# Kernel optimization log

Hardware: AMD Instinct MI355X
Metric: run time of the kernel (lower is better)

Reference implementation:

```python
import jax, jax.numpy as jnp
import numpy as np

V, OOV, E, HE, HD, B, S, T = 50000, 100, 128, 256, 256, 32, 256, 16
NEG = -1e20


def lstm(x, W, U, b, h0, c0):
    # x: [B, L, F]; standard (Keras-style i,f,g,o) LSTM via scan over time
    def step(carry, xt):
        h, c = carry
        z = xt @ W + h @ U + b
        i, f, g, o = jnp.split(z, 4, axis=-1)
        c = jax.nn.sigmoid(f) * c + jax.nn.sigmoid(i) * jnp.tanh(g)
        h = jax.nn.sigmoid(o) * jnp.tanh(c)
        return (h, c), h
    (h, c), hs = jax.lax.scan(step, (h0, c0), jnp.swapaxes(x, 0, 1))
    return jnp.swapaxes(hs, 0, 1), h, c


def setup_inputs() -> dict:
    key = jax.random.key(0)
    ks = jax.random.split(key, 16)
    g = lambda i, shape: jax.random.normal(ks[i], shape, dtype=jnp.float32) * 0.05
    return {
        'x': jax.random.randint(ks[0], (B, S), 0, V),
        'x_with_oov': jax.random.randint(ks[1], (B, S), 0, V + OOV),
        'x_len': jax.random.randint(ks[2], (B,), 1, S + 1),
        'dec_x': jax.random.randint(ks[3], (B, T), 0, V),
        'embedding': g(4, (V, E)),
        'Wenc': g(5, (E, 4 * HE)), 'Uenc': g(6, (HE, 4 * HE)), 'benc': jnp.zeros(4 * HE, jnp.float32),
        'We2d': g(7, (HE, HD)), 'be2d': jnp.zeros(HD, jnp.float32),
        'Wdec': g(8, (E, 4 * HD)), 'Udec': g(9, (HD, 4 * HD)), 'bdec': jnp.zeros(4 * HD, jnp.float32),
        'Wattn': g(10, (HD, HE)),
        'Wout': g(11, (HE + HD, HD)), 'bout': jnp.zeros(HD, jnp.float32),
        'Wgen': g(12, (HD, V)),
        'Wcopy': g(13, (HE, HD)), 'bcopy': jnp.zeros(HD, jnp.float32),
    }


def reference(x, x_with_oov, x_len, dec_x, embedding, Wenc, Uenc, benc,
              We2d, be2d, Wdec, Udec, bdec, Wattn, Wout, bout, Wgen, Wcopy, bcopy):
    # Encoder (unidirectional; Keras encoder ignores mask in this branch)
    enc_out, eh, ec = lstm(embedding[x], Wenc, Uenc, benc,
                           jnp.zeros((B, HE), embedding.dtype), jnp.zeros((B, HE), embedding.dtype))
    # NOTE: source applies encoder2decoder_state to BOTH h and c (faithful)
    h0 = eh @ We2d + be2d
    c0 = ec @ We2d + be2d
    # Decoder LSTM
    dec_out, sh, sc = lstm(embedding[dec_x], Wdec, Udec, bdec, h0, c0)  # [B,T,HD]
    mask = jnp.arange(S)[None, :] < x_len[:, None]                      # [B,S]
    # Attention (score_mode='general')
    scores = jnp.einsum('bth,he,bse->bts', dec_out, Wattn, enc_out)     # [B,T,S]
    scores = jnp.where(mask[:, None, :], scores, NEG)
    aw = jax.nn.softmax(scores, axis=2)
    ctx = jnp.einsum('bts,bse->bte', aw, enc_out)                       # [B,T,HE]
    attn_out = jnp.tanh(jnp.concatenate([ctx, dec_out], axis=-1) @ Wout + bout)  # [B,T,HD]
    # Generation scores, padded with tiny constant over OOV slots
    gen = jnp.exp(attn_out @ Wgen)                                      # [B,T,V]
    gen = jnp.pad(gen, ((0, 0), (0, 0), (0, OOV)), constant_values=1e-10)
    # Copy scores over source positions, scattered into extended vocab
    copy_seq = jnp.einsum('bsh,bth->bts', jnp.tanh(enc_out @ Wcopy + bcopy), attn_out)
    copy_seq = jnp.exp(jnp.where(mask[:, None, :], copy_seq, NEG))      # [B,T,S]
    b_idx = jnp.arange(B)[:, None, None]
    t_idx = jnp.arange(T)[None, :, None]
    v_idx = x_with_oov[:, None, :]                                      # broadcast to [B,T,S]
    copy_vocab = jnp.zeros((B, T, V + OOV), gen.dtype).at[b_idx, t_idx, v_idx].add(copy_seq)
    total = gen + copy_vocab
    log_prob = jnp.log(total / jnp.sum(total, axis=2, keepdims=True))
    return log_prob, sh, sc
```

## Files before the change

kernel.cpp:

```cpp
#include <hip/hip_runtime.h>

#define V_   50000
#define OOV_ 100
#define VO_  50100
#define E_   128
#define HE_  256
#define HD_  256
#define B_   32
#define S_   256
#define T_   16

typedef _Float16 h2_t __attribute__((ext_vector_type(2)));
typedef __attribute__((ext_vector_type(8))) short bfrag_t;
typedef __attribute__((ext_vector_type(4))) float f32x4;
typedef unsigned short ushort_t;

union U32H2 { unsigned u; h2_t h; };
union FRAG  { uint4 u; bfrag_t s; };

static __device__ __forceinline__ float bf2f(unsigned short b) {
  return __uint_as_float(((unsigned)b) << 16);
}
static __device__ __forceinline__ unsigned short f2bf(float f) {
  unsigned u = __float_as_uint(f);
  unsigned r = (u + 0x7fffu + ((u >> 16) & 1u)) >> 16;
  return (unsigned short)r;
}
static __device__ __forceinline__ float sigm(float x) { return 1.f / (1.f + expf(-x)); }
static __device__ __forceinline__ float fast_sigm(float z) {
  float e = __builtin_amdgcn_exp2f(-1.442695041f * z);
  return __builtin_amdgcn_rcpf(1.f + e);
}
static __device__ __forceinline__ float fast_tanh(float z) {
  float e = __builtin_amdgcn_exp2f(-2.885390082f * z);
  return 2.f * __builtin_amdgcn_rcpf(1.f + e) - 1.f;
}

static __device__ __forceinline__ float dot2u(unsigned upair, unsigned hpairv, float acc) {
  U32H2 a; a.u = upair;
  U32H2 b; b.u = hpairv;
#if __has_builtin(__builtin_amdgcn_fdot2)
  return __builtin_amdgcn_fdot2(a.h, b.h, acc, false);
#else
  acc = fmaf((float)a.h.x, (float)b.h.x, acc);
  return fmaf((float)a.h.y, (float)b.h.y, acc);
#endif
}

__global__ __launch_bounds__(256) void mfma_gemm(
    const ushort_t* __restrict__ A, const ushort_t* __restrict__ Bt,
    const float* __restrict__ bias, float* __restrict__ C, ushort_t* __restrict__ Cbf,
    float* __restrict__ rsum, int M, int N, int K, int ldC, int act)
{
  const int w = threadIdx.x >> 6, lane = threadIdx.x & 63;
  const int m0 = blockIdx.y * 64 + w * 16;
  const int n0 = blockIdx.x * 64;
  const int l16 = lane & 15, lq = lane >> 4;
  f32x4 acc[4] = {f32x4{0,0,0,0}, f32x4{0,0,0,0}, f32x4{0,0,0,0}, f32x4{0,0,0,0}};
  for (int k0 = 0; k0 < K; k0 += 32) {
    FRAG a;
    a.u = *(const uint4*)(A + (size_t)(m0 + l16) * K + k0 + lq * 8);
#pragma unroll
    for (int ns = 0; ns < 4; ns++) {
      int n = n0 + ns * 16 + l16;
      int nc = n < N ? n : N - 1;
      FRAG bf;
      bf.u = *(const uint4*)(Bt + (size_t)nc * K + k0 + lq * 8);
      acc[ns] = __builtin_amdgcn_mfma_f32_16x16x32_bf16(a.s, bf.s, acc[ns], 0, 0, 0);
    }
  }
  float bv[4];
#pragma unroll
  for (int ns = 0; ns < 4; ns++) {
    int col = n0 + ns * 16 + l16;
    bv[ns] = (bias && col < N) ? bias[col] : 0.f;
  }
#pragma unroll
  for (int r = 0; r < 4; r++) {
    int row = m0 + lq * 4 + r;
    float part = 0.f;
#pragma unroll
    for (int ns = 0; ns < 4; ns++) {
      int col = n0 + ns * 16 + l16;
      if (col < N) {
        float v = acc[ns][r] + bv[ns];
        if (act == 1) v = tanhf(v);
        else if (act == 2) v = expf(v);
        if (Cbf) Cbf[(size_t)row * ldC + col] = f2bf(v);
        else     C[(size_t)row * ldC + col] = v;
        part += v;
      }
    }
    if (rsum) {
      part += __shfl_xor(part, 1);
      part += __shfl_xor(part, 2);
      part += __shfl_xor(part, 4);
      part += __shfl_xor(part, 8);
      if (l16 == 0) atomicAdd(&rsum[row], part);
    }
  }
}

__global__ __launch_bounds__(256) void wgen_gemm(
    const ushort_t* __restrict__ A, const float* __restrict__ Wg,
    float* __restrict__ out, float* __restrict__ rsum)
{
  __shared__ ushort_t ldsB[64 * 264];
  const int tid = threadIdx.x;
  const int n0 = blockIdx.x * 64;
#pragma unroll
  for (int it = 0; it < 16; it++) {
    int idx = it * 256 + tid;
    int k = idx >> 4, c4 = idx & 15;
    int nsrc = n0 + c4 * 4;
    if (nsrc > V_ - 4) nsrc = V_ - 4;
    float4 f = *(const float4*)&Wg[(size_t)k * V_ + nsrc];
    ldsB[(c4 * 4 + 0) * 264 + k] = f2bf(f.x);
    ldsB[(c4 * 4 + 1) * 264 + k] = f2bf(f.y);
    ldsB[(c4 * 4 + 2) * 264 + k] = f2bf(f.z);
    ldsB[(c4 * 4 + 3) * 264 + k] = f2bf(f.w);
  }
  __syncthreads();
  const int w = tid >> 6, lane = tid & 63;
  const int l16 = lane & 15, lq = lane >> 4;
  for (int mt = 0; mt < 8; mt++) {
    const int mb = mt * 64 + w * 16;
    f32x4 acc[4] = {f32x4{0,0,0,0}, f32x4{0,0,0,0}, f32x4{0,0,0,0}, f32x4{0,0,0,0}};
#pragma unroll
    for (int k0 = 0; k0 < 256; k0 += 32) {
      FRAG a;
      a.u = *(const uint4*)(A + (size_t)(mb + l16) * 256 + k0 + lq * 8);
#pragma unroll
      for (int ns = 0; ns < 4; ns++) {
        FRAG bf;
        bf.u = *(const uint4*)&ldsB[(ns * 16 + l16) * 264 + k0 + lq * 8];
        acc[ns] = __builtin_amdgcn_mfma_f32_16x16x32_bf16(a.s, bf.s, acc[ns], 0, 0, 0);
      }
    }
#pragma unroll
    for (int r = 0; r < 4; r++) {
      int row = mb + lq * 4 + r;
      float part = 0.f;
#pragma unroll
      for (int ns = 0; ns < 4; ns++) {
        int col = n0 + ns * 16 + l16;
        if (col < V_) {
          float v = expf(acc[ns][r]);
          out[(size_t)row * VO_ + col] = v;
          part += v;
        }
      }
      part += __shfl_xor(part, 1);
      part += __shfl_xor(part, 2);
      part += __shfl_xor(part, 4);
      part += __shfl_xor(part, 8);
      if (l16 == 0) atomicAdd(&rsum[row], part);
    }
  }
}

static __device__ __forceinline__ void tconv_tile(
    const float* __restrict__ W, ushort_t* __restrict__ Wt, int K, int N,
    int kb, int nb, int tid, ushort_t (*tile)[33])
{
  const int tx = tid & 31, ty = tid >> 5;
#pragma unroll
  for (int p = 0; p < 4; p++) {
    int k = kb + ty + p * 8, n = nb + tx;
    if (k < K && n < N) tile[ty + p * 8][tx] = f2bf(W[(size_t)k * N + n]);
  }
  __syncthreads();
#pragma unroll
  for (int p = 0; p < 4; p++) {
    int n = nb + ty + p * 8, k = kb + tx;
    if (k < K && n < N) Wt[(size_t)n * K + k] = tile[tx][ty + p * 8];
  }
}
static __device__ __forceinline__ void packU2_one(
    const float* __restrict__ U, unsigned* __restrict__ out, int i)
{
  int p = i >> 10, col = i & 1023;
  U32H2 cv; cv.h = h2_t{(_Float16)U[(size_t)(2 * p) * 1024 + col],
                        (_Float16)U[(size_t)(2 * p + 1) * 1024 + col]};
  out[i] = cv.u;
}

__global__ __launch_bounds__(256) void prep_kernel(
    const float* __restrict__ Wenc, const float* __restrict__ Wdec,
    const float* __restrict__ We2d, const float* __restrict__ Wattn,
    const float* __restrict__ Wout, const float* __restrict__ Wcopy,
    const float* __restrict__ Uenc, const float* __restrict__ Udec,
    const int* __restrict__ x, const int* __restrict__ decx, const float* __restrict__ emb,
    ushort_t* WencT, ushort_t* WdecT, ushort_t* We2dT, ushort_t* WattnT,
    ushort_t* WoutT, ushort_t* WcopyT, unsigned* Upk2E, unsigned* Upk2D,
    ushort_t* xembbf, ushort_t* dembbf)
{
  __shared__ ushort_t tile[32][33];
  int blk = blockIdx.x;
  const int tid = threadIdx.x;
  if (blk < 128) { tconv_tile(Wenc, WencT, 128, 1024, (blk >> 5) * 32, (blk & 31) * 32, tid, tile); return; }
  blk -= 128;
  if (blk < 128) { tconv_tile(Wdec, WdecT, 128, 1024, (blk >> 5) * 32, (blk & 31) * 32, tid, tile); return; }
  blk -= 128;
  if (blk < 64)  { tconv_tile(We2d, We2dT, 256, 256, (blk >> 3) * 32, (blk & 7) * 32, tid, tile); return; }
  blk -= 64;
  if (blk < 64)  { tconv_tile(Wattn, WattnT, 256, 256, (blk >> 3) * 32, (blk & 7) * 32, tid, tile); return; }
  blk -= 64;
  if (blk < 128) { tconv_tile(Wout, WoutT, 512, 256, (blk >> 3) * 32, (blk & 7) * 32, tid, tile); return; }
  blk -= 128;
  if (blk < 64)  { tconv_tile(Wcopy, WcopyT, 256, 256, (blk >> 3) * 32, (blk & 7) * 32, tid, tile); return; }
  blk -= 64;
  if (blk < 512) { packU2_one(Uenc, Upk2E, blk * 256 + tid); return; }
  blk -= 512;
  if (blk < 512) { packU2_one(Udec, Upk2D, blk * 256 + tid); return; }
  blk -= 512;
  if (blk < 4096) {
    int i = blk * 256 + tid, r = i >> 7;
    xembbf[i] = f2bf(emb[(size_t)x[r] * E_ + (i & 127)]);
    return;
  }
  blk -= 4096;
  {
    int i = blk * 256 + tid, r = i >> 7;
    dembbf[i] = f2bf(emb[(size_t)decx[r] * E_ + (i & 127)]);
  }
}

#define DOT8(u0, u1, hpi)                \
  acc[0] = dot2u(u0.x, hpi, acc[0]);     \
  acc[1] = dot2u(u0.y, hpi, acc[1]);     \
  acc[2] = dot2u(u0.z, hpi, acc[2]);     \
  acc[3] = dot2u(u0.w, hpi, acc[3]);     \
  acc[4] = dot2u(u1.x, hpi, acc[4]);     \
  acc[5] = dot2u(u1.y, hpi, acc[5]);     \
  acc[6] = dot2u(u1.z, hpi, acc[6]);     \
  acc[7] = dot2u(u1.w, hpi, acc[7]);

__global__
__attribute__((amdgpu_flat_work_group_size(1024, 1024), amdgpu_waves_per_eu(4, 4)))
void lstm12(
    const float* __restrict__ Xpre, const unsigned* __restrict__ Upk2,
    const float* __restrict__ h0, const float* __restrict__ c0,
    ushort_t* __restrict__ outH, float* __restrict__ hN, float* __restrict__ cN,
    ushort_t* __restrict__ hNbf, ushort_t* __restrict__ cNbf,
    int steps)
{
  __shared__ unsigned ldsU[8 * 4096];
  __shared__ float    zpart[4 * 1028];
  __shared__ unsigned hpair[8 * 20];
  const int tid = threadIdx.x;

  const int b = blockIdx.x;
  const int jg = tid >> 3, kq = tid & 7;

  uint4 Ur[24];
  const unsigned* ubase = Upk2 + jg * 8;
#pragma unroll
  for (int i = 0; i < 12; i++) {
    int p = kq * 16 + i;
    Ur[2 * i]     = *(const uint4*)(ubase + p * 1024);
    Ur[2 * i + 1] = *(const uint4*)(ubase + p * 1024 + 4);
  }
  {
    unsigned* myst = &ldsU[tid * 4];
#pragma unroll
    for (int i = 0; i < 4; i++) {
      int p = kq * 16 + 12 + i;
      uint4 q0 = *(const uint4*)(ubase + p * 1024);
      uint4 q1 = *(const uint4*)(ubase + p * 1024 + 4);
      *(uint4*)(myst + (2 * i) * 4096)     = q0;
      *(uint4*)(myst + (2 * i + 1) * 4096) = q1;
    }
  }
  float c = 0.f, hcur = 0.f;
  if (tid < 256) {
    c    = c0 ? c0[b * 256 + tid] : 0.f;
    hcur = h0 ? h0[b * 256 + tid] : 0.f;
  }
  if (tid < 128) {
    float a  = h0 ? h0[b * 256 + 2 * tid] : 0.f;
    float b2 = h0 ? h0[b * 256 + 2 * tid + 1] : 0.f;
    U32H2 cv; cv.h = h2_t{(_Float16)a, (_Float16)b2};
    hpair[(tid >> 4) * 20 + (tid & 15)] = cv.u;
  }
  __syncthreads();

  const float* xp = Xpre + (size_t)b * steps * 1024;
  const unsigned* myld = &ldsU[tid * 4];

  for (int t = 0; t < steps; t++) {
    float xq0 = 0.f, xq1 = 0.f, xq2 = 0.f, xq3 = 0.f;
    if (tid < 256) {
      const float* xr = xp + (size_t)t * 1024 + tid;
      xq0 = xr[0]; xq1 = xr[256]; xq2 = xr[512]; xq3 = xr[768];
    }
    float acc[8] = {0.f, 0.f, 0.f, 0.f, 0.f, 0.f, 0.f, 0.f};
    {
      uint4 hA = *(const uint4*)&hpair[kq * 20];
      DOT8(Ur[0], Ur[1], hA.x)  DOT8(Ur[2], Ur[3], hA.y)
      DOT8(Ur[4], Ur[5], hA.z)  DOT8(Ur[6], Ur[7], hA.w)
    }
    {
      uint4 hB = *(const uint4*)&hpair[kq * 20 + 4];
      DOT8(Ur[8], Ur[9], hB.x)   DOT8(Ur[10], Ur[11], hB.y)
      DOT8(Ur[12], Ur[13], hB.z) DOT8(Ur[14], Ur[15], hB.w)
    }
    {
      uint4 hC = *(const uint4*)&hpair[kq * 20 + 8];
      DOT8(Ur[16], Ur[17], hC.x) DOT8(Ur[18], Ur[19], hC.y)
      DOT8(Ur[20], Ur[21], hC.z) DOT8(Ur[22], Ur[23], hC.w)
    }
    {
      uint4 hD = *(const uint4*)&hpair[kq * 20 + 12];
      unsigned hh[4] = {hD.x, hD.y, hD.z, hD.w};
#pragma unroll
      for (int r = 0; r < 4; r++) {
        uint4 u0 = *(const uint4*)(myld + (2 * r) * 4096);
        uint4 u1 = *(const uint4*)(myld + (2 * r + 1) * 4096);
        unsigned hpi = hh[r];
        DOT8(u0, u1, hpi)
      }
    }
#pragma unroll
    for (int g = 0; g < 8; g++) acc[g] += __shfl_xor(acc[g], 1);
    if ((kq & 1) == 0) {
      int r = kq >> 1;
      *(float4*)&zpart[r * 1028 + jg * 8]     = make_float4(acc[0], acc[1], acc[2], acc[3]);
      *(float4*)&zpart[r * 1028 + jg * 8 + 4] = make_float4(acc[4], acc[5], acc[6], acc[7]);
    }
    __syncthreads();
    if (tid < 256) {
      float zi = xq0, zf = xq1, zg = xq2, zo = xq3;
#pragma unroll
      for (int r = 0; r < 4; r++) {
        const float* zr = &zpart[r * 1028 + tid];
        zi += zr[0]; zf += zr[256]; zg += zr[512]; zo += zr[768];
      }
      float ai = fast_sigm(zi), af = fast_sigm(zf);
      float ag = fast_tanh(zg), ao = fast_sigm(zo);
      c = fmaf(af, c, ai * ag);
      hcur = ao * fast_tanh(c);
      outH[((size_t)b * steps + t) * 256 + tid] = f2bf(hcur);
      float hnx = __shfl_down(hcur, 1);
      if ((tid & 1) == 0) {
        U32H2 cv; cv.h = h2_t{(_Float16)hcur, (_Float16)hnx};
        int P = tid >> 1;
        hpair[(P >> 4) * 20 + (P & 15)] = cv.u;
      }
    }
    __syncthreads();
  }
  if (tid < 256) {
    if (hN)   hN[b * 256 + tid] = hcur;
    if (cN)   cN[b * 256 + tid] = c;
    if (hNbf) hNbf[b * 256 + tid] = f2bf(hcur);
    if (cNbf) cNbf[b * 256 + tid] = f2bf(c);
  }
}

__global__ __launch_bounds__(256) void attn_kernel(
    const float* __restrict__ dq, const ushort_t* __restrict__ enc,
    const int* __restrict__ x_len, const ushort_t* __restrict__ dec,
    ushort_t* __restrict__ catb)
{
  __shared__ float q[256];
  __shared__ float eb[32][256];
  __shared__ float sc[256];
  __shared__ float red[8];
  const int bt = blockIdx.x, tid = threadIdx.x;
  const int b = bt >> 4;
  q[tid] = dq[(size_t)bt * 256 + tid];
  const int len = x_len[b];
  const unsigned* encu = (const unsigned*)(enc + (size_t)b * S_ * 256);
  __syncthreads();
  const int s_loc = tid >> 3, hb = (tid & 7) * 32;
  for (int cch = 0; cch < 8; cch++) {
#pragma unroll
    for (int qv = 0; qv < 16; qv++) {
      int idx = qv * 256 + tid;
      unsigned u = encu[cch * 4096 + idx];
      int row = idx >> 7, cp2 = (idx & 127) * 2;
      eb[row][cp2]     = bf2f((unsigned short)(u & 0xffffu));
      eb[row][cp2 + 1] = bf2f((unsigned short)(u >> 16));
    }
    __syncthreads();
    float p = 0.f;
#pragma unroll
    for (int h = 0; h < 32; h++) p = fmaf(q[hb + h], eb[s_loc][hb + h], p);
    p += __shfl_down(p, 4, 8);
    p += __shfl_down(p, 2, 8);
    p += __shfl_down(p, 1, 8);
    if ((tid & 7) == 0) sc[cch * 32 + s_loc] = p;
    __syncthreads();
  }
  float my = (tid < len) ? sc[tid] : -1e30f;
  float m = my;
#pragma unroll
  for (int o = 32; o >= 1; o >>= 1) m = fmaxf(m, __shfl_xor(m, o));
  if ((tid & 63) == 0) red[tid >> 6] = m;
  __syncthreads();
  float bm = fmaxf(fmaxf(red[0], red[1]), fmaxf(red[2], red[3]));
  float e = expf(my - bm);
  float s = e;
#pragma unroll
  for (int o = 32; o >= 1; o >>= 1) s += __shfl_xor(s, o);
  if ((tid & 63) == 0) red[4 + (tid >> 6)] = s;
  __syncthreads();
  float tot = red[4] + red[5] + red[6] + red[7];
  sc[tid] = e / tot;
  __syncthreads();
  const ushort_t* encb = enc + (size_t)b * S_ * 256;
  float acc = 0.f;
  for (int s2 = 0; s2 < 256; s2++) acc = fmaf(sc[s2], bf2f(encb[(size_t)s2 * 256 + tid]), acc);
  catb[(size_t)bt * 512 + tid]       = f2bf(acc);
  catb[(size_t)bt * 512 + 256 + tid] = dec[(size_t)bt * 256 + tid];
}

__global__ __launch_bounds__(256) void copyseq_kernel(
    const ushort_t* __restrict__ at, const ushort_t* __restrict__ cp,
    const int* __restrict__ x_len, float* __restrict__ cseq)
{
  __shared__ float q[256];
  __shared__ float eb[32][256];
  __shared__ float sc[256];
  const int bt = blockIdx.x, tid = threadIdx.x;
  const int b = bt >> 4;
  q[tid] = bf2f(at[(size_t)bt * 256 + tid]);
  const int len = x_len[b];
  const unsigned* cpu_ = (const unsigned*)(cp + (size_t)b * S_ * 256);
  __syncthreads();
  const int s_loc = tid >> 3, hb = (tid & 7) * 32;
  for (int cch = 0; cch < 8; cch++) {
#pragma unroll
    for (int qv = 0; qv < 16; qv++) {
      int idx = qv * 256 + tid;
      unsigned u = cpu_[cch * 4096 + idx];
      int row = idx >> 7, cp2 = (idx & 127) * 2;
      eb[row][cp2]     = bf2f((unsigned short)(u & 0xffffu));
      eb[row][cp2 + 1] = bf2f((unsigned short)(u >> 16));
    }
    __syncthreads();
    float p = 0.f;
#pragma unroll
    for (int h = 0; h < 32; h++) p = fmaf(q[hb + h], eb[s_loc][hb + h], p);
    p += __shfl_down(p, 4, 8);
    p += __shfl_down(p, 2, 8);
    p += __shfl_down(p, 1, 8);
    if ((tid & 7) == 0) sc[cch * 32 + s_loc] = p;
    __syncthreads();
  }
  cseq[(size_t)bt * 256 + tid] = (tid < len) ? expf(sc[tid]) : 0.f;
}

__global__ __launch_bounds__(256) void scatter_kernel(
    const float* __restrict__ cseq, const int* __restrict__ xoov,
    float* __restrict__ out, float* __restrict__ rsum)
{
  __shared__ float red[4];
  const int bt = blockIdx.x, tid = threadIdx.x, b = bt >> 4;
  if (tid < OOV_) out[(size_t)bt * VO_ + V_ + tid] = 1e-10f;
  __syncthreads();
  float v = cseq[(size_t)bt * 256 + tid];
  if (v != 0.f) atomicAdd(&out[(size_t)bt * VO_ + xoov[b * S_ + tid]], v);
  float s = v;
#pragma unroll
  for (int o = 32; o >= 1; o >>= 1) s += __shfl_xor(s, o);
  if ((tid & 63) == 0) red[tid >> 6] = s;
  __syncthreads();
  if (tid == 0) atomicAdd(&rsum[bt], red[0] + red[1] + red[2] + red[3]);
}
__global__ void rowlog_kernel(const float* __restrict__ rsum, float* __restrict__ rowlog) {
  int i = blockIdx.x * 256 + threadIdx.x;
  if (i < B_ * T_) rowlog[i] = logf(rsum[i] + 1e-8f);
}
__global__ void finalize_kernel(float* __restrict__ out, const float* __restrict__ rowlog) {
  size_t i = (size_t)blockIdx.x * 256 + threadIdx.x;
  if (i < (size_t)B_ * T_ * VO_) {
    int bt = (int)(i / VO_);
    out[i] = logf(out[i]) - rowlog[bt];
  }
}

extern "C" void kernel_launch(void* const* d_in, const int* in_sizes, int n_in,
                              void* d_out, int out_size, void* d_ws, size_t ws_size,
                              hipStream_t stream) {
  const int*   x     = (const int*)d_in[0];
  const int*   xoov  = (const int*)d_in[1];
  const int*   xlen  = (const int*)d_in[2];
  const int*   decx  = (const int*)d_in[3];
  const float* emb   = (const float*)d_in[4];
  const float* Wenc  = (const float*)d_in[5];
  const float* Uenc  = (const float*)d_in[6];
  const float* benc  = (const float*)d_in[7];
  const float* We2d  = (const float*)d_in[8];
  const float* be2d  = (const float*)d_in[9];
  const float* Wdec  = (const float*)d_in[10];
  const float* Udec  = (const float*)d_in[11];
  const float* bdec  = (const float*)d_in[12];
  const float* Wattn = (const float*)d_in[13];
  const float* Wout  = (const float*)d_in[14];
  const float* bout  = (const float*)d_in[15];
  const float* Wgen  = (const float*)d_in[16];
  const float* Wcopy = (const float*)d_in[17];
  const float* bcopy = (const float*)d_in[18];
  float* out = (float*)d_out;
  float* ws  = (float*)d_ws;

  float*    Xenc   = ws + 0;
  ushort_t* cp_bf  = (ushort_t*)(ws + 6400000);
  float*    dqb    = ws + 8388608;
  float*    cseq   = ws + 8781824;
  float*    rsum   = ws + 8912896;
  float*    rowlog = ws + 8913408;
  ushort_t* Abf    = (ushort_t*)(ws + 8913920);
  ushort_t* catb   = (ushort_t*)(ws + 8979456);
  ushort_t* decObf = (ushort_t*)(ws + 9110528);
  ushort_t* xembbf = (ushort_t*)(ws + 9176064);
  ushort_t* dembbf = (ushort_t*)(ws + 9700352);
  float*    Xdec   = ws + 9733120;
  ushort_t* WencT  = (ushort_t*)(ws + 10257408);
  ushort_t* WdecT  = (ushort_t*)(ws + 10322944);
  ushort_t* We2dT  = (ushort_t*)(ws + 10388480);
  ushort_t* WattnT = (ushort_t*)(ws + 10421248);
  ushort_t* WoutT  = (ushort_t*)(ws + 10454016);
  ushort_t* WcopyT = (ushort_t*)(ws + 10519552);
  unsigned* Upk2E  = (unsigned*)(ws + 10552320);
  unsigned* Upk2D  = (unsigned*)(ws + 10683392);
  ushort_t* encObf = (ushort_t*)(ws + 10814464);
  ushort_t* ehcbf  = (ushort_t*)(ws + 11879424);
  float*    h0c0   = ws + 11887616;

  float* sh  = out + (size_t)B_ * T_ * VO_;
  float* scf = sh + B_ * HD_;

  hipMemsetAsync(rsum, 0, 512 * sizeof(float), stream);

  hipLaunchKernelGGL(prep_kernel, dim3(5952), dim3(256), 0, stream,
                     Wenc, Wdec, We2d, Wattn, Wout, Wcopy, Uenc, Udec, x, decx, emb,
                     WencT, WdecT, We2dT, WattnT, WoutT, WcopyT, Upk2E, Upk2D,
                     xembbf, dembbf);

  hipLaunchKernelGGL(mfma_gemm, dim3(16, 128), dim3(256), 0, stream,
                     xembbf, WencT, benc, Xenc, (ushort_t*)nullptr, (float*)nullptr,
                     B_ * S_, 1024, 128, 1024, 0);
  hipLaunchKernelGGL(mfma_gemm, dim3(16, 8), dim3(256), 0, stream,
                     dembbf, WdecT, bdec, Xdec, (ushort_t*)nullptr, (float*)nullptr,
                     B_ * T_, 1024, 128, 1024, 0);

  hipLaunchKernelGGL(lstm12, dim3(32), dim3(1024), 0, stream,
                     Xenc, Upk2E, (const float*)nullptr, (const float*)nullptr,
                     encObf, (float*)nullptr, (float*)nullptr,
                     ehcbf, ehcbf + 32 * 256, S_);

  hipLaunchKernelGGL(mfma_gemm, dim3(4, 1), dim3(256), 0, stream,
                     ehcbf, We2dT, be2d, h0c0, (ushort_t*)nullptr, (float*)nullptr,
                     64, 256, 256, 256, 0);

  hipLaunchKernelGGL(lstm12, dim3(32), dim3(1024), 0, stream,
                     Xdec, Upk2D, h0c0, h0c0 + 32 * 256, decObf, sh, scf,
                     (ushort_t*)nullptr, (ushort_t*)nullptr, T_);

  hipLaunchKernelGGL(mfma_gemm, dim3(4, 8), dim3(256), 0, stream,
                     decObf, WattnT, (const float*)nullptr, dqb, (ushort_t*)nullptr,
                     (float*)nullptr, B_ * T_, 256, 256, 256, 0);
  hipLaunchKernelGGL(attn_kernel, dim3(B_ * T_), dim3(256), 0, stream,
                     dqb, encObf, xlen, decObf, catb);
  hipLaunchKernelGGL(mfma_gemm, dim3(4, 8), dim3(256), 0, stream,
                     catb, WoutT, bout, (float*)nullptr, Abf, (float*)nullptr,
                     B_ * T_, 256, 512, 256, 1);
  hipLaunchKernelGGL(mfma_gemm, dim3(4, 128), dim3(256), 0, stream,
                     encObf, WcopyT, bcopy, (float*)nullptr, cp_bf, (float*)nullptr,
                     B_ * S_, 256, 256, 256, 1);
  hipLaunchKernelGGL(wgen_gemm, dim3(782), dim3(256), 0, stream,
                     Abf, Wgen, out, rsum);
  hipLaunchKernelGGL(copyseq_kernel, dim3(B_ * T_), dim3(256), 0, stream, Abf, cp_bf, xlen, cseq);
  hipLaunchKernelGGL(scatter_kernel, dim3(512), dim3(256), 0, stream, cseq, xoov, out, rsum);
  hipLaunchKernelGGL(rowlog_kernel, dim3(2), dim3(256), 0, stream, rsum, rowlog);
  hipLaunchKernelGGL(finalize_kernel, dim3((B_ * T_ * VO_ + 255) / 256), dim3(256), 0, stream,
                     out, rowlog);
}
```

Before: 1.105 ms.

## Overlap copy GEMM with decoder LSTM, fuse attention query, skip masked positions

Extra thread blocks are added to the decoder LSTM launch. They compute the tanh(enc@Wcopy+b) GEMM with MFMA, so that work runs on CUs the 32 serial LSTM blocks leave idle and its separate launch goes away. The Wattn query projection moves into the attention kernel, which removes another GEMM launch and the dq buffer. Attention and copy-score loops now stop at each row's x_len, skipping masked source chunks. The finalize log pass uses float4 accesses. In exchange, the extra blocks run at the LSTM's 1024-thread, large-LDS configuration, and the per-block query projection is scalar FMA work.

```diff
diff --git a/kernel.cpp b/kernel.cpp
--- a/kernel.cpp
+++ b/kernel.cpp
@@ -243,12 +243,45 @@
     const float* __restrict__ h0, const float* __restrict__ c0,
     ushort_t* __restrict__ outH, float* __restrict__ hN, float* __restrict__ cN,
     ushort_t* __restrict__ hNbf, ushort_t* __restrict__ cNbf,
-    int steps)
+    int steps,
+    const ushort_t* __restrict__ encA, const ushort_t* __restrict__ WcT,
+    const float* __restrict__ bcp, ushort_t* __restrict__ cpout)
 {
   __shared__ unsigned ldsU[8 * 4096];
   __shared__ float    zpart[4 * 1028];
   __shared__ unsigned hpair[8 * 20];
   const int tid = threadIdx.x;
+
+  if (blockIdx.x >= 32) {
+    int tb = blockIdx.x - 32;
+    const int n0 = (tb & 3) * 64;
+    const int mt = tb >> 2;
+    const int w = tid >> 6, lane = tid & 63;
+    const int l16 = lane & 15, lq = lane >> 4;
+    const int m0 = mt * 256 + w * 16;
+    f32x4 acc[4] = {f32x4{0,0,0,0}, f32x4{0,0,0,0}, f32x4{0,0,0,0}, f32x4{0,0,0,0}};
+#pragma unroll
+    for (int k0 = 0; k0 < 256; k0 += 32) {
+      FRAG a;
+      a.u = *(const uint4*)(encA + (size_t)(m0 + l16) * 256 + k0 + lq * 8);
+#pragma unroll
+      for (int ns = 0; ns < 4; ns++) {
+        FRAG bf;
+        bf.u = *(const uint4*)(WcT + (size_t)(n0 + ns * 16 + l16) * 256 + k0 + lq * 8);
+        acc[ns] = __builtin_amdgcn_mfma_f32_16x16x32_bf16(a.s, bf.s, acc[ns], 0, 0, 0);
+      }
+    }
+#pragma unroll
+    for (int r = 0; r < 4; r++) {
+      int row = m0 + lq * 4 + r;
+#pragma unroll
+      for (int ns = 0; ns < 4; ns++) {
+        int col = n0 + ns * 16 + l16;
+        cpout[(size_t)row * 256 + col] = f2bf(tanhf(acc[ns][r] + bcp[col]));
+      }
+    }
+    return;
+  }
 
   const int b = blockIdx.x;
   const int jg = tid >> 3, kq = tid & 7;
@@ -359,22 +392,44 @@
 }
 
 __global__ __launch_bounds__(256) void attn_kernel(
-    const float* __restrict__ dq, const ushort_t* __restrict__ enc,
-    const int* __restrict__ x_len, const ushort_t* __restrict__ dec,
+    const ushort_t* __restrict__ dec, const ushort_t* __restrict__ WattnT,
+    const ushort_t* __restrict__ enc, const int* __restrict__ x_len,
     ushort_t* __restrict__ catb)
 {
   __shared__ float q[256];
+  __shared__ float decf[256];
   __shared__ float eb[32][256];
   __shared__ float sc[256];
   __shared__ float red[8];
   const int bt = blockIdx.x, tid = threadIdx.x;
   const int b = bt >> 4;
-  q[tid] = dq[(size_t)bt * 256 + tid];
   const int len = x_len[b];
+  if (tid < 128) {
+    unsigned u = ((const unsigned*)(dec + (size_t)bt * 256))[tid];
+    decf[2 * tid]     = bf2f((unsigned short)(u & 0xffffu));
+    decf[2 * tid + 1] = bf2f((unsigned short)(u >> 16));
+  }
+  __syncthreads();
+  {
+    const ushort_t* wrow = WattnT + (size_t)tid * 256;
+    float acc = 0.f;
+#pragma unroll 4
+    for (int k0 = 0; k0 < 256; k0 += 8) {
+      uint4 wv = *(const uint4*)(wrow + k0);
+      unsigned ws[4] = {wv.x, wv.y, wv.z, wv.w};
+#pragma unroll
+      for (int e = 0; e < 4; e++) {
+        acc = fmaf(decf[k0 + 2 * e],     bf2f((unsigned short)(ws[e] & 0xffffu)), acc);
+        acc = fmaf(decf[k0 + 2 * e + 1], bf2f((unsigned short)(ws[e] >> 16)),     acc);
+      }
+    }
+    q[tid] = acc;
+  }
+  __syncthreads();
   const unsigned* encu = (const unsigned*)(enc + (size_t)b * S_ * 256);
-  __syncthreads();
   const int s_loc = tid >> 3, hb = (tid & 7) * 32;
-  for (int cch = 0; cch < 8; cch++) {
+  const int nch = (len + 31) >> 5;
+  for (int cch = 0; cch < nch; cch++) {
 #pragma unroll
     for (int qv = 0; qv < 16; qv++) {
       int idx = qv * 256 + tid;
@@ -411,7 +466,7 @@
   __syncthreads();
   const ushort_t* encb = enc + (size_t)b * S_ * 256;
   float acc = 0.f;
-  for (int s2 = 0; s2 < 256; s2++) acc = fmaf(sc[s2], bf2f(encb[(size_t)s2 * 256 + tid]), acc);
+  for (int s2 = 0; s2 < len; s2++) acc = fmaf(sc[s2], bf2f(encb[(size_t)s2 * 256 + tid]), acc);
   catb[(size_t)bt * 512 + tid]       = f2bf(acc);
   catb[(size_t)bt * 512 + 256 + tid] = dec[(size_t)bt * 256 + tid];
 }
@@ -430,7 +485,8 @@
   const unsigned* cpu_ = (const unsigned*)(cp + (size_t)b * S_ * 256);
   __syncthreads();
   const int s_loc = tid >> 3, hb = (tid & 7) * 32;
-  for (int cch = 0; cch < 8; cch++) {
+  const int nch = (len + 31) >> 5;
+  for (int cch = 0; cch < nch; cch++) {
 #pragma unroll
     for (int qv = 0; qv < 16; qv++) {
       int idx = qv * 256 + tid;
@@ -474,10 +530,16 @@
   if (i < B_ * T_) rowlog[i] = logf(rsum[i] + 1e-8f);
 }
 __global__ void finalize_kernel(float* __restrict__ out, const float* __restrict__ rowlog) {
-  size_t i = (size_t)blockIdx.x * 256 + threadIdx.x;
-  if (i < (size_t)B_ * T_ * VO_) {
-    int bt = (int)(i / VO_);
-    out[i] = logf(out[i]) - rowlog[bt];
+  size_t i4 = ((size_t)blockIdx.x * 256 + threadIdx.x) * 4;
+  if (i4 < (size_t)B_ * T_ * VO_) {
+    int bt = (int)(i4 / VO_);
+    float rl = rowlog[bt];
+    float4 v = *(float4*)&out[i4];
+    v.x = logf(v.x) - rl;
+    v.y = logf(v.y) - rl;
+    v.z = logf(v.z) - rl;
+    v.w = logf(v.w) - rl;
+    *(float4*)&out[i4] = v;
   }
 }
 
@@ -508,7 +570,6 @@
 
   float*    Xenc   = ws + 0;
   ushort_t* cp_bf  = (ushort_t*)(ws + 6400000);
-  float*    dqb    = ws + 8388608;
   float*    cseq   = ws + 8781824;
   float*    rsum   = ws + 8912896;
   float*    rowlog = ws + 8913408;
@@ -550,32 +611,29 @@
   hipLaunchKernelGGL(lstm12, dim3(32), dim3(1024), 0, stream,
                      Xenc, Upk2E, (const float*)nullptr, (const float*)nullptr,
                      encObf, (float*)nullptr, (float*)nullptr,
-                     ehcbf, ehcbf + 32 * 256, S_);
+                     ehcbf, ehcbf + 32 * 256, S_,
+                     (const ushort_t*)nullptr, (const ushort_t*)nullptr,
+                     (const float*)nullptr, (ushort_t*)nullptr);
 
   hipLaunchKernelGGL(mfma_gemm, dim3(4, 1), dim3(256), 0, stream,
                      ehcbf, We2dT, be2d, h0c0, (ushort_t*)nullptr, (float*)nullptr,
                      64, 256, 256, 256, 0);
 
-  hipLaunchKernelGGL(lstm12, dim3(32), dim3(1024), 0, stream,
+  hipLaunchKernelGGL(lstm12, dim3(32 + 128), dim3(1024), 0, stream,
                      Xdec, Upk2D, h0c0, h0c0 + 32 * 256, decObf, sh, scf,
-                     (ushort_t*)nullptr, (ushort_t*)nullptr, T_);
-
-  hipLaunchKernelGGL(mfma_gemm, dim3(4, 8), dim3(256), 0, stream,
-                     decObf, WattnT, (const float*)nullptr, dqb, (ushort_t*)nullptr,
-                     (float*)nullptr, B_ * T_, 256, 256, 256, 0);
+                     (ushort_t*)nullptr, (ushort_t*)nullptr, T_,
+                     encObf, WcopyT, bcopy, cp_bf);
+
   hipLaunchKernelGGL(attn_kernel, dim3(B_ * T_), dim3(256), 0, stream,
-                     dqb, encObf, xlen, decObf, catb);
+                     decObf, WattnT, encObf, xlen, catb);
   hipLaunchKernelGGL(mfma_gemm, dim3(4, 8), dim3(256), 0, stream,
                      catb, WoutT, bout, (float*)nullptr, Abf, (float*)nullptr,
                      B_ * T_, 256, 512, 256, 1);
-  hipLaunchKernelGGL(mfma_gemm, dim3(4, 128), dim3(256), 0, stream,
-                     encObf, WcopyT, bcopy, (float*)nullptr, cp_bf, (float*)nullptr,
-                     B_ * S_, 256, 256, 256, 1);
   hipLaunchKernelGGL(wgen_gemm, dim3(782), dim3(256), 0, stream,
                      Abf, Wgen, out, rsum);
   hipLaunchKernelGGL(copyseq_kernel, dim3(B_ * T_), dim3(256), 0, stream, Abf, cp_bf, xlen, cseq);
   hipLaunchKernelGGL(scatter_kernel, dim3(512), dim3(256), 0, stream, cseq, xoov, out, rsum);
   hipLaunchKernelGGL(rowlog_kernel, dim3(2), dim3(256), 0, stream, rsum, rowlog);
-  hipLaunchKernelGGL(finalize_kernel, dim3((B_ * T_ * VO_ + 255) / 256), dim3(256), 0, stream,
+  hipLaunchKernelGGL(finalize_kernel, dim3((B_ * T_ * VO_ / 4 + 255) / 256), dim3(256), 0, stream,
                      out, rowlog);
 }
```

Result: faster. 1.044 ms (-5.5%).
